# Performance work log

Measured on AMD Instinct MI355X. Metric: run time of the kernel, lower is better.

The kernel has to match this reference:

```python
import jax, jax.numpy as jnp
import numpy as np
from jax import lax

# ---- constants matching init kwargs / proposal_creator(mode='testing') ----
RATIOS = (0.5, 1.0, 2.0)
SCALES = (8.0, 16.0, 32.0)
BASE = 16.0          # generate_anchor_base base_size
STRIDE = 16          # feat_stride
NMS_THRESH = 0.7
N_PRE = 3000         # n_test_pre_nms
N_POST = 300         # n_test_post_nms
MIN_SIZE = 16.0      # min_size * scale (scale=1)


def _anchor_base():
    # (9, 4) xyxy anchors centered at (BASE/2, BASE/2); ratios outer, scales inner
    r = np.array(RATIOS, np.float32)
    s = np.array(SCALES, np.float32)
    hs = (BASE * s[None, :] * np.sqrt(r)[:, None]).reshape(-1)
    ws = (BASE * s[None, :] * np.sqrt(1.0 / r)[:, None]).reshape(-1)
    cx = cy = BASE / 2.0
    return np.stack([cx - ws / 2, cy - hs / 2, cx + ws / 2, cy + hs / 2], 1).astype(np.float32)


def _all_anchors(h, w):
    # _enumerate_shifted_anchor: shift grid flattened y-outer/x-inner to match
    # permute(0,2,3,1).view(n,-1,4) layout of the conv outputs.
    base = jnp.asarray(_anchor_base())                     # (9,4)
    sx = jnp.arange(w, dtype=jnp.float32) * STRIDE
    sy = jnp.arange(h, dtype=jnp.float32) * STRIDE
    SX, SY = jnp.meshgrid(sx, sy)                          # (h,w)
    shifts = jnp.stack([SX, SY, SX, SY], -1).reshape(-1, 4)  # (h*w,4)
    return (shifts[:, None, :] + base[None, :, :]).reshape(-1, 4)  # (h*w*9,4)


def _proposals(loc, score, anchor, img_h, img_w):
    # loc: (K,4) deltas, score: (K,) fg prob, anchor: (K,4) xyxy
    aw = anchor[:, 2] - anchor[:, 0]
    ah = anchor[:, 3] - anchor[:, 1]
    acx = anchor[:, 0] + 0.5 * aw
    acy = anchor[:, 1] + 0.5 * ah
    cx = loc[:, 0] * aw + acx
    cy = loc[:, 1] * ah + acy
    bw = aw * jnp.exp(loc[:, 2])
    bh = ah * jnp.exp(loc[:, 3])
    x1 = jnp.clip(cx - 0.5 * bw, 0.0, img_w)
    y1 = jnp.clip(cy - 0.5 * bh, 0.0, img_h)
    x2 = jnp.clip(cx + 0.5 * bw, 0.0, img_w)
    y2 = jnp.clip(cy + 0.5 * bh, 0.0, img_h)
    boxes = jnp.stack([x1, y1, x2, y2], 1)
    valid = ((x2 - x1) >= MIN_SIZE) & ((y2 - y1) >= MIN_SIZE)
    # min-size filter -> sink invalid boxes with -inf score, then top-k pre-NMS
    masked = jnp.where(valid, score, -jnp.inf)
    _, idx = lax.top_k(masked, N_PRE)
    b = boxes[idx]                                         # (N_PRE,4), score-sorted desc
    v = valid[idx]
    # pairwise IoU (torchvision convention: no +1)
    area = (b[:, 2] - b[:, 0]) * (b[:, 3] - b[:, 1])
    ix1 = jnp.maximum(b[:, None, 0], b[None, :, 0])
    iy1 = jnp.maximum(b[:, None, 1], b[None, :, 1])
    ix2 = jnp.minimum(b[:, None, 2], b[None, :, 2])
    iy2 = jnp.minimum(b[:, None, 3], b[None, :, 3])
    inter = jnp.clip(ix2 - ix1, 0.0) * jnp.clip(iy2 - iy1, 0.0)
    union = area[:, None] + area[None, :] - inter
    iou = jnp.where(union > 0.0, inter / union, 0.0)
    sup = iou > NMS_THRESH                                 # (N_PRE,N_PRE) bool
    # greedy sequential NMS over score order
    ar = jnp.arange(N_PRE)
    def body(keep, i):
        keep = keep & ~(keep[i] & sup[i] & (ar > i))
        return keep, None
    keep, _ = lax.scan(body, v, ar)
    # first N_POST kept boxes (score order); pad by cycling kept boxes
    order = jnp.argsort(jnp.where(keep, ar, N_PRE))        # kept indices first, sorted
    nk = jnp.maximum(keep.sum(), 1)
    pos = jnp.arange(N_POST)
    sel = order[jnp.where(pos < nk, pos, pos % nk)]
    return b[sel]                                          # (N_POST,4)


def setup_inputs() -> dict:
    key = jax.random.key(0)
    ks = jax.random.split(key, 4)
    n, c, h, w = 4, 512, 38, 38
    return {
        "x": jax.random.normal(ks[0], (n, c, h, w), jnp.float32),
        "conv1_w": jax.random.normal(ks[1], (512, 512, 3, 3), jnp.float32) * 0.01,
        "conv1_b": jnp.zeros((512,), jnp.float32),
        "score_w": jax.random.normal(ks[2], (18, 512), jnp.float32) * 0.01,
        "score_b": jnp.zeros((18,), jnp.float32),
        "loc_w": jax.random.normal(ks[3], (36, 512), jnp.float32) * 0.01,
        "loc_b": jnp.zeros((36,), jnp.float32),
        "img_h": 608,
        "img_w": 608,
    }


def reference(x, conv1_w, conv1_b, score_w, score_b, loc_w, loc_b, img_h, img_w):
    n, _, h, w = x.shape
    feat = jax.nn.relu(
        lax.conv_general_dilated(x, conv1_w, (1, 1), "SAME",
                                 dimension_numbers=("NCHW", "OIHW", "NCHW"))
        + conv1_b[None, :, None, None])
    locs = jnp.einsum("nchw,oc->nohw", feat, loc_w) + loc_b[None, :, None, None]
    scores = jnp.einsum("nchw,oc->nohw", feat, score_w) + score_b[None, :, None, None]
    rpn_locs = locs.transpose(0, 2, 3, 1).reshape(n, -1, 4)      # (n, h*w*9, 4)
    rpn_scores = scores.transpose(0, 2, 3, 1).reshape(n, -1, 2)  # (n, h*w*9, 2)
    fg = jax.nn.softmax(rpn_scores, axis=-1)[..., 1]             # (n, h*w*9)
    anchor = _all_anchors(h, w)
    ih = jnp.float32(img_h)
    iw = jnp.float32(img_w)
    rois = jax.vmap(lambda l, s: _proposals(l, s, anchor, ih, iw))(rpn_locs, fg)
    rois_indices = jnp.broadcast_to(
        jnp.arange(n, dtype=x.dtype)[:, None], (n, N_POST))
    return rpn_locs, rpn_scores, rois.reshape(-1, 4), rois_indices, anchor[None]
```

## Files before the change

kernel.cpp:

```cpp
#include <hip/hip_runtime.h>
#include <cstdint>
#include <cstddef>

#define HW    1444
#define NA    12996
#define NPRE  3000
#define NW    47
#define NPOST 300

#define OFF_LOCS   0
#define OFF_SCORES 207936
#define OFF_ROIS   311904
#define OFF_IDX    316704
#define OFF_ANCH   317904

#define INVALID_KEY 0xFFF0000000000000ULL

typedef float f32x2 __attribute__((ext_vector_type(2)));
typedef float f32x4 __attribute__((ext_vector_type(4)));

__device__ inline double as_dim(int raw) {
  if (raw > 0 && raw < 1000000) return (double)raw;
  return (double)__int_as_float(raw);
}

__global__ __launch_bounds__(256) void wt_k(const float* __restrict__ lw,
                                            const float* __restrict__ sw,
                                            float* __restrict__ Wt) {
  int t = blockIdx.x * 256 + threadIdx.x;
  if (t >= 64 * 512) return;
  int o = t & 63, c = t >> 6;
  float v = 0.f;
  if (o < 36)      v = lw[o * 512 + c];
  else if (o < 54) v = sw[(o - 36) * 512 + c];
  Wt[t] = v;
}

__global__ __launch_bounds__(256) void conv_k(const float* __restrict__ X,
                                              const float* __restrict__ W,
                                              const float* __restrict__ B,
                                              float* __restrict__ F) {
  __shared__ float Xs[1008];
  __shared__ float Wsf[2304];
  const int tid  = threadIdx.x;
  const int lane = tid & 63;
  const int wv   = tid >> 6;
  const int seg  = wv * 10;
  const int y  = blockIdx.x;
  const int o0 = blockIdx.y * 64;
  const int n  = blockIdx.z;
  const float* xn = X + ((size_t)n * 512) * HW;

  int xsrcA[2]; bool xvalA[2]; bool xactA1;
  {
    int e = tid;
    int cl = e / 120, rem = e - cl * 120, row = rem / 40, colA = rem - row * 40;
    int m = colA - 1, iy = y - 1 + row;
    xvalA[0] = (m >= 0 && m < 38 && iy >= 0 && iy < 38);
    xsrcA[0] = xvalA[0] ? (cl * HW + iy * 38 + m) : 0;
  }
  {
    int e = tid + 256; xactA1 = (e < 480);
    int cl = e / 120, rem = e - cl * 120, row = rem / 40, colA = rem - row * 40;
    int m = colA - 1, iy = y - 1 + row;
    xvalA[1] = xactA1 && (m >= 0 && m < 38 && iy >= 0 && iy < 38);
    xsrcA[1] = xvalA[1] ? (cl * HW + iy * 38 + m) : 0;
  }
  int xsrcB[3]; bool xvalB[3]; bool xactB2;
#pragma unroll
  for (int u = 0; u < 3; ++u) {
    int e = tid + u * 256;
    bool act = (e < 528);
    int cl = e / 132, rem = e - cl * 132, row = rem / 44, colB = rem - row * 44;
    int m = colB - 3, iy = y - 1 + row;
    xvalB[u] = act && (m >= 0 && m < 38 && iy >= 0 && iy < 38);
    xsrcB[u] = xvalB[u] ? (cl * HW + iy * 38 + m) : 0;
    if (u == 2) xactB2 = act;
  }
  int wsrc[9];
#pragma unroll
  for (int u = 0; u < 9; ++u) {
    int e = tid + u * 256;
    int ol = e / 36, t36 = e - ol * 36;
    wsrc[u] = (o0 + ol) * 4608 + t36;
  }

  float xrA[2], xrB[3], wr_[9];
#pragma unroll
  for (int u = 0; u < 2; ++u) xrA[u] = xvalA[u] ? xn[xsrcA[u]] : 0.f;
#pragma unroll
  for (int u = 0; u < 3; ++u) xrB[u] = xvalB[u] ? xn[xsrcB[u]] : 0.f;
#pragma unroll
  for (int u = 0; u < 9; ++u) wr_[u] = W[wsrc[u]];

  double acc[10];
#pragma unroll
  for (int p = 0; p < 10; ++p) acc[p] = 0.;
  f32x2 pA[5], pB[5];
  float pc0 = 0.f;

  const int  xb0   = (wv & 1) ? (480 + seg + 2) : seg;
  const int  cstep = (wv & 1) ? 132 : 120;
  const int  kstep = (wv & 1) ? 44 : 40;

#define WQ_ELEM(t) ((t & 3) == 0 ? wq[(t) >> 2].x : (t & 3) == 1 ? wq[(t) >> 2].y : \
                    (t & 3) == 2 ? wq[(t) >> 2].z : wq[(t) >> 2].w)

  for (int cc = 0; cc < 128; ++cc) {
    __syncthreads();
    Xs[tid] = xrA[0];
    if (xactA1) Xs[tid + 256] = xrA[1];
    Xs[480 + tid] = xrB[0];
    Xs[480 + tid + 256] = xrB[1];
    if (xactB2) Xs[480 + tid + 512] = xrB[2];
#pragma unroll
    for (int u = 0; u < 9; ++u) Wsf[tid + u * 256] = wr_[u];
    __syncthreads();
    if (cc < 127) {
      const int cb = (cc + 1) * 4;
#pragma unroll
      for (int u = 0; u < 2; ++u) xrA[u] = xvalA[u] ? xn[cb * HW + xsrcA[u]] : 0.f;
#pragma unroll
      for (int u = 0; u < 3; ++u) xrB[u] = xvalB[u] ? xn[cb * HW + xsrcB[u]] : 0.f;
#pragma unroll
      for (int u = 0; u < 9; ++u) wr_[u] = W[wsrc[u] + (cc + 1) * 36];
    }
    f32x4 wq[9];
    {
      const f32x4* wrow = (const f32x4*)&Wsf[lane * 36];
#pragma unroll
      for (int q = 0; q < 9; ++q) wq[q] = wrow[q];
    }
    if ((cc & 1) == 0) {
#pragma unroll
      for (int a = 0; a < 5; ++a) { pA[a] = (f32x2)(0.f); pB[a] = (f32x2)(0.f); }
      pc0 = 0.f;
    }
#pragma unroll
    for (int cl = 0; cl < 4; ++cl) {
      f32x2 wp[9];
#pragma unroll
      for (int k = 0; k < 9; ++k) {
        float wv0 = WQ_ELEM(cl * 9 + k);
        wp[k][0] = wv0; wp[k][1] = wv0;
      }
#pragma unroll
      for (int ky = 0; ky < 3; ++ky) {
        const float* xrow = &Xs[xb0 + cl * cstep + ky * kstep];
        f32x4 q0 = *(const f32x4*)(xrow);
        f32x4 q1 = *(const f32x4*)(xrow + 4);
        f32x4 q2 = *(const f32x4*)(xrow + 8);
        f32x2 xp[6];
        xp[0] = __builtin_shufflevector(q0, q0, 0, 1);
        xp[1] = __builtin_shufflevector(q0, q0, 2, 3);
        xp[2] = __builtin_shufflevector(q1, q1, 0, 1);
        xp[3] = __builtin_shufflevector(q1, q1, 2, 3);
        xp[4] = __builtin_shufflevector(q2, q2, 0, 1);
        xp[5] = __builtin_shufflevector(q2, q2, 2, 3);
#pragma unroll
        for (int a = 0; a < 5; ++a)
          asm("v_pk_fma_f32 %0, %1, %2, %0"
              : "+v"(pA[a]) : "v"(xp[a]), "v"(wp[ky * 3 + 0]));
        pc0 = fmaf(wp[ky * 3 + 1][0], xp[0][1], pc0);
#pragma unroll
        for (int a = 0; a < 5; ++a)
          asm("v_pk_fma_f32 %0, %1, %2, %0"
              : "+v"(pB[a]) : "v"(xp[a + 1]), "v"(wp[ky * 3 + 1]));
#pragma unroll
        for (int a = 0; a < 5; ++a)
          asm("v_pk_fma_f32 %0, %1, %2, %0"
              : "+v"(pA[a]) : "v"(xp[a + 1]), "v"(wp[ky * 3 + 2]));
      }
    }
    if (cc & 1) {
      acc[0] += (double)(pA[0][0] + pc0);
#pragma unroll
      for (int p = 1; p < 10; ++p) {
        float sa = pA[p >> 1][p & 1];
        float sb = (p & 1) ? pB[(p - 1) >> 1][0] : pB[(p - 2) >> 1][1];
        acc[p] += (double)(sa + sb);
      }
    }
  }
  double bb = (double)B[o0 + lane];
  float* fp = F + ((size_t)(n * 512 + o0 + lane)) * HW + y * 38;
#pragma unroll
  for (int p = 0; p < 10; ++p) {
    int col = seg + p;
    if (col < 38) fp[col] = (float)fmax(acc[p] + bb, 0.0);
  }
}

__global__ __launch_bounds__(256) void heads_k(const float* __restrict__ F,
                                               const float* __restrict__ Wt,
                                               const float* __restrict__ lb,
                                               const float* __restrict__ sb,
                                               float* __restrict__ out,
                                               double* __restrict__ fg) {
  __shared__ float sf[512 * 4];
  __shared__ double ssc[4][18];
  int n = blockIdx.y;
  int p0 = blockIdx.x * 4;
  int tid = threadIdx.x;
  const float* fn = F + ((size_t)n * 512) * HW;
  for (int e = tid; e < 2048; e += 256) {
    int c = e >> 2, pl = e & 3;
    sf[e] = fn[c * HW + p0 + pl];
  }
  __syncthreads();
  int pl = tid & 3, o = tid >> 2;
  double acc = 0.;
  if (o < 54) {
    for (int c = 0; c < 512; ++c)
      acc = fma((double)Wt[(c << 6) | o], (double)sf[(c << 2) | pl], acc);
  }
  int p = p0 + pl;
  if (o < 36) {
    acc += (double)lb[o];
    out[OFF_LOCS + ((size_t)n * NA + (size_t)p * 9 + (o >> 2)) * 4 + (o & 3)] = (float)acc;
  } else if (o < 54) {
    int oo = o - 36;
    acc += (double)sb[oo];
    out[OFF_SCORES + ((size_t)n * NA + (size_t)p * 9 + (oo >> 1)) * 2 + (oo & 1)] = (float)acc;
    ssc[pl][oo] = acc;
  }
  __syncthreads();
  if (tid < 36) {
    int pl2 = tid / 9, a = tid - pl2 * 9;
    double s0 = ssc[pl2][a * 2], s1 = ssc[pl2][a * 2 + 1];
    double mx = fmax(s0, s1);
    double e0 = exp(s0 - mx), e1 = exp(s1 - mx);
    fg[(size_t)n * NA + (size_t)(p0 + pl2) * 9 + a] = e1 / (e0 + e1);
  }
}

__global__ __launch_bounds__(256) void decode_k(const float* __restrict__ out_c,
                                                float* __restrict__ out,
                                                const double* __restrict__ fg,
                                                const int* __restrict__ ihp,
                                                const int* __restrict__ iwp,
                                                double* __restrict__ boxes,
                                                unsigned long long* __restrict__ keys) {
  int t = blockIdx.x * 256 + threadIdx.x;
  int n = t >> 14, i = t & 16383;
  if (i >= NA) { keys[t] = ~0ULL; return; }
  int p = i / 9, a = i - p * 9;
  int ri = a / 3, si = a - ri * 3;
  double sr  = (ri == 0) ? 0.7071067811865476 : (ri == 1 ? 1.0 : 1.4142135623730951);
  double sri = (ri == 0) ? 1.4142135623730951 : (ri == 1 ? 1.0 : 0.7071067811865476);
  double hs = (double)(128 << si) * sr;
  double wd = (double)(128 << si) * sri;
  int py = p / 38, px = p - py * 38;
  float sx = (float)(px * 16), sy = (float)(py * 16);
  float fx1 = (float)(8.0 - 0.5 * wd), fy1 = (float)(8.0 - 0.5 * hs);
  float fx2 = (float)(8.0 + 0.5 * wd), fy2 = (float)(8.0 + 0.5 * hs);
  float ax1f = sx + fx1, ay1f = sy + fy1, ax2f = sx + fx2, ay2f = sy + fy2;
  if (n == 0) {
    float* ap = out + OFF_ANCH + (size_t)i * 4;
    ap[0] = ax1f; ap[1] = ay1f; ap[2] = ax2f; ap[3] = ay2f;
  }
  double ax1 = ax1f, ay1 = ay1f, ax2 = ax2f, ay2 = ay2f;
  double aw = ax2 - ax1, ah = ay2 - ay1;
  double acx = ax1 + 0.5 * aw, acy = ay1 + 0.5 * ah;
  const float* lp = out_c + OFF_LOCS + ((size_t)n * NA + i) * 4;
  double cx = (double)lp[0] * aw + acx, cy = (double)lp[1] * ah + acy;
  double bw = aw * exp((double)lp[2]), bh = ah * exp((double)lp[3]);
  double iwf = as_dim(iwp[0]), ihf = as_dim(ihp[0]);
  double x1 = fmin(fmax(cx - 0.5 * bw, 0.0), iwf);
  double y1 = fmin(fmax(cy - 0.5 * bh, 0.0), ihf);
  double x2 = fmin(fmax(cx + 0.5 * bw, 0.0), iwf);
  double y2 = fmin(fmax(cy + 0.5 * bh, 0.0), ihf);
  bool valid = ((x2 - x1) >= 16.0) && ((y2 - y1) >= 16.0);
  double* bp = boxes + ((size_t)n * NA + i) * 4;
  bp[0] = x1; bp[1] = y1; bp[2] = x2; bp[3] = y2;
  double sc = fg[(size_t)n * NA + i];
  unsigned long long u = (unsigned long long)__double_as_longlong(sc);
  u = (u >> 63) ? ~u : (u | 0x8000000000000000ULL);
  unsigned long long inv = ~u;
  if (!valid) inv = INVALID_KEY;
  keys[t] = (inv & ~0x3FFFULL) | (unsigned long long)i;
}

__global__ __launch_bounds__(1024) void sortA_k(unsigned long long* __restrict__ keys) {
  __shared__ unsigned long long s[8192];
  const int half = blockIdx.x & 1;
  unsigned long long* g = keys + (((size_t)(blockIdx.x >> 1)) << 14) + ((size_t)half << 13);
  const int tid = threadIdx.x;
  for (int i = tid; i < 8192; i += 1024) s[i] = g[i];
  for (int size = 2; size <= 8192; size <<= 1) {
    for (int stride = size >> 1; stride > 0; stride >>= 1) {
      __syncthreads();
      for (int u = tid; u < 4096; u += 1024) {
        int lo = u & (stride - 1);
        int i1 = ((u - lo) << 1) | lo;
        int i2 = i1 + stride;
        bool up = (i1 & size) == 0;
        if (half) up = !up;
        unsigned long long a = s[i1], b = s[i2];
        if ((a > b) == up) { s[i1] = b; s[i2] = a; }
      }
    }
  }
  __syncthreads();
  for (int i = tid; i < 8192; i += 1024) g[i] = s[i];
}

__global__ __launch_bounds__(256) void sortB_k(unsigned long long* __restrict__ keys) {
  int t = blockIdx.x * 256 + threadIdx.x;
  int n = t >> 13, i = t & 8191;
  unsigned long long* g = keys + ((size_t)n << 14);
  unsigned long long a = g[i], b = g[i + 8192];
  if (a > b) { g[i] = b; g[i + 8192] = a; }
}

__global__ __launch_bounds__(1024) void sortC_k(unsigned long long* __restrict__ keys) {
  __shared__ unsigned long long s[8192];
  unsigned long long* g = keys + (((size_t)(blockIdx.x >> 1)) << 14) + ((size_t)(blockIdx.x & 1) << 13);
  const int tid = threadIdx.x;
  for (int i = tid; i < 8192; i += 1024) s[i] = g[i];
  for (int stride = 4096; stride > 0; stride >>= 1) {
    __syncthreads();
    for (int u = tid; u < 4096; u += 1024) {
      int lo = u & (stride - 1);
      int i1 = ((u - lo) << 1) | lo;
      int i2 = i1 + stride;
      unsigned long long a = s[i1], b = s[i2];
      if (a > b) { s[i1] = b; s[i2] = a; }
    }
  }
  __syncthreads();
  for (int i = tid; i < 8192; i += 1024) g[i] = s[i];
}

__global__ void gather_k(const unsigned long long* __restrict__ keys,
                         const double* __restrict__ boxes,
                         double* __restrict__ bsort,
                         unsigned long long* __restrict__ vw) {
  int n = blockIdx.y, w = blockIdx.x, l = threadIdx.x;
  int r = w * 64 + l;
  bool valid = false;
  if (r < NPRE) {
    unsigned long long kk = keys[((size_t)n << 14) + r];
    valid = kk < INVALID_KEY;
    unsigned idx = (unsigned)(kk & 0x3FFFULL);
    const double* bp = boxes + ((size_t)n * NA + idx) * 4;
    double* dp = bsort + ((size_t)n * NPRE + r) * 4;
    dp[0] = bp[0]; dp[1] = bp[1]; dp[2] = bp[2]; dp[3] = bp[3];
  }
  unsigned long long mask = __ballot(valid);
  if (l == 0) vw[n * NW + w] = mask;
}

__global__ __launch_bounds__(256) void iou_k(const double* __restrict__ bsort,
                                             unsigned long long* __restrict__ sup) {
  int t = blockIdx.x * 256 + threadIdx.x;
  if (t >= 4 * NPRE * NW) return;
  int w = t % NW; int rest = t / NW; int i = rest % NPRE; int n = rest / NPRE;
  const double* bb = bsort + (size_t)n * NPRE * 4;
  double bix1 = bb[(size_t)i*4], biy1 = bb[(size_t)i*4+1];
  double bix2 = bb[(size_t)i*4+2], biy2 = bb[(size_t)i*4+3];
  double ai = (bix2 - bix1) * (biy2 - biy1);
  unsigned long long word = 0ULL;
  int j0 = w << 6;
  if (j0 + 63 > i) {
    int lmax = NPRE - j0; if (lmax > 64) lmax = 64;
    for (int l = 0; l < lmax; ++l) {
      int j = j0 + l;
      if (j <= i) continue;
      const double* bj = bb + (size_t)j * 4;
      double aj = (bj[2] - bj[0]) * (bj[3] - bj[1]);
      double xx1 = fmax(bix1, bj[0]), yy1 = fmax(biy1, bj[1]);
      double xx2 = fmin(bix2, bj[2]), yy2 = fmin(biy2, bj[3]);
      double inter = fmax(xx2 - xx1, 0.0) * fmax(yy2 - yy1, 0.0);
      double uni = ai + aj - inter;
      double iou = (uni > 0.0) ? inter / uni : 0.0;
      word |= (unsigned long long)(iou > 0.7) << l;
    }
  }
  sup[((size_t)n * NPRE + i) * NW + w] = word;
}

__global__ void nms_k(const unsigned long long* __restrict__ sup,
                      const unsigned long long* __restrict__ vwp,
                      const double* __restrict__ bsort,
                      float* __restrict__ out) {
  int n = blockIdx.x; int l = threadIdx.x;
  unsigned long long vw = (l < NW) ? vwp[n * NW + l] : 0ULL;
  unsigned long long remv = 0ULL, keepw = 0ULL;
  const unsigned long long* sbase = sup + (size_t)n * NPRE * NW;
  unsigned long long r = (l < NPRE) ? sbase[(size_t)l * NW] : 0ULL;
  for (int b = 0; b < NW; ++b) {
    unsigned long long rn = 0ULL;
    if (b + 1 < NW) {
      int gi = (b + 1) * 64 + l;
      if (gi < NPRE) rn = sbase[(size_t)gi * NW + (b + 1)];
    }
    unsigned long long kept = __shfl(vw & ~remv, b);
    unsigned long long todo = kept;
    while (todo) {
      int i = __builtin_ctzll(todo);
      unsigned long long ri = __shfl(r, i);
      kept &= ~ri;
      todo &= todo - 1;
      todo &= ~ri;
    }
    if (l == b) keepw = kept;
    unsigned long long m = kept;
    while (m) {
      int i0 = __builtin_ctzll(m); m &= m - 1;
      int i1 = -1, i2 = -1, i3 = -1, i4 = -1, i5 = -1, i6 = -1, i7 = -1;
      if (m) { i1 = __builtin_ctzll(m); m &= m - 1; }
      if (m) { i2 = __builtin_ctzll(m); m &= m - 1; }
      if (m) { i3 = __builtin_ctzll(m); m &= m - 1; }
      if (m) { i4 = __builtin_ctzll(m); m &= m - 1; }
      if (m) { i5 = __builtin_ctzll(m); m &= m - 1; }
      if (m) { i6 = __builtin_ctzll(m); m &= m - 1; }
      if (m) { i7 = __builtin_ctzll(m); m &= m - 1; }
      if (l < NW) {
        const unsigned long long* rb = sbase + (size_t)(b << 6) * NW + l;
        unsigned long long a0 = rb[(size_t)i0 * NW];
        unsigned long long a1 = (i1 >= 0) ? rb[(size_t)i1 * NW] : 0ULL;
        unsigned long long a2 = (i2 >= 0) ? rb[(size_t)i2 * NW] : 0ULL;
        unsigned long long a3 = (i3 >= 0) ? rb[(size_t)i3 * NW] : 0ULL;
        unsigned long long a4 = (i4 >= 0) ? rb[(size_t)i4 * NW] : 0ULL;
        unsigned long long a5 = (i5 >= 0) ? rb[(size_t)i5 * NW] : 0ULL;
        unsigned long long a6 = (i6 >= 0) ? rb[(size_t)i6 * NW] : 0ULL;
        unsigned long long a7 = (i7 >= 0) ? rb[(size_t)i7 * NW] : 0ULL;
        remv |= (((a0 | a1) | (a2 | a3)) | ((a4 | a5) | (a6 | a7)));
      }
    }
    r = rn;
  }
  unsigned long long keep = keepw;
  int cnt = __popcll(keep);
  int pre = cnt;
#pragma unroll
  for (int d = 1; d < 64; d <<= 1) {
    int tt = __shfl_up(pre, d);
    if (l >= d) pre += tt;
  }
  int nk = __shfl(pre, 63);
  int excl = pre - cnt;
  __shared__ float sbox[NPOST * 4];
  unsigned long long m2 = keep; int rank = excl;
  while (m2) {
    int b = __builtin_ctzll(m2);
    m2 &= m2 - 1;
    if (rank < NPOST) {
      int j = (l << 6) + b;
      const double* bj = bsort + ((size_t)n * NPRE + j) * 4;
      sbox[rank*4]   = (float)bj[0]; sbox[rank*4+1] = (float)bj[1];
      sbox[rank*4+2] = (float)bj[2]; sbox[rank*4+3] = (float)bj[3];
    }
    ++rank;
  }
  __syncthreads();
  if (nk == 0 && l == 0) {
    const double* b0 = bsort + (size_t)n * NPRE * 4;
    sbox[0] = (float)b0[0]; sbox[1] = (float)b0[1];
    sbox[2] = (float)b0[2]; sbox[3] = (float)b0[3];
  }
  __syncthreads();
  int nke = nk > 0 ? nk : 1;
  for (int r2 = l; r2 < NPOST; r2 += 64) {
    int src = r2 < nke ? r2 : r2 % nke;
    float4 b4 = *(float4*)(sbox + src * 4);
    *(float4*)(out + OFF_ROIS + ((size_t)n * NPOST + r2) * 4) = b4;
    out[OFF_IDX + n * NPOST + r2] = (float)n;
  }
}

extern "C" void kernel_launch(void* const* d_in, const int* in_sizes, int n_in,
                              void* d_out, int out_size, void* d_ws, size_t ws_size,
                              hipStream_t stream) {
  const float* X  = (const float*)d_in[0];
  const float* CW = (const float*)d_in[1];
  const float* CB = (const float*)d_in[2];
  const float* SW = (const float*)d_in[3];
  const float* SB = (const float*)d_in[4];
  const float* LW = (const float*)d_in[5];
  const float* LB = (const float*)d_in[6];
  const int*   IH = (const int*)d_in[7];
  const int*   IW = (const int*)d_in[8];
  float* out = (float*)d_out;
  char* ws = (char*)d_ws;

  float* feat = (float*)(ws + 0);
  unsigned long long* sup  = (unsigned long long*)(ws + 0);
  float* Wt    = (float*)(ws + 11829248);
  double* fg   = (double*)(ws + 11960320);
  double* boxes= (double*)(ws + 12376192);
  unsigned long long* keys = (unsigned long long*)(ws + 14039680);
  double* bsort= (double*)(ws + 14563968);
  unsigned long long* vw   = (unsigned long long*)(ws + 14947968);

  hipLaunchKernelGGL(wt_k,     dim3(128),        dim3(256),  0, stream, LW, SW, Wt);
  hipLaunchKernelGGL(conv_k,   dim3(38, 8, 4),   dim3(256),  0, stream, X, CW, CB, feat);
  hipLaunchKernelGGL(heads_k,  dim3(361, 4),     dim3(256),  0, stream, feat, Wt, LB, SB, out, fg);
  hipLaunchKernelGGL(decode_k, dim3(256),        dim3(256),  0, stream, out, out, fg, IH, IW, boxes, keys);
  hipLaunchKernelGGL(sortA_k,  dim3(8),          dim3(1024), 0, stream, keys);
  hipLaunchKernelGGL(sortB_k,  dim3(128),        dim3(256),  0, stream, keys);
  hipLaunchKernelGGL(sortC_k,  dim3(8),          dim3(1024), 0, stream, keys);
  hipLaunchKernelGGL(gather_k, dim3(47, 4),      dim3(64),   0, stream, keys, boxes, bsort, vw);
  hipLaunchKernelGGL(iou_k,    dim3((4*NPRE*NW + 255) / 256), dim3(256), 0, stream, bsort, sup);
  hipLaunchKernelGGL(nms_k,    dim3(4),          dim3(64),   0, stream, sup, vw, bsort, out);
}
```

Baseline: 980.2 us.

## Fuse decode into heads, merge sort stages with gather, drop IoU division

The box decode and key generation now run in the heads kernel's epilogue, reading locs from shared memory instead of launching a separate decode kernel. Key padding moves into the weight-transpose kernel. The bitonic merge step, final half-sort and gather are combined into one kernel: it keeps only the smaller half of each merged pair, sorts it, and gathers the top boxes from shared memory. The IoU test compares inter against 0.7*union instead of dividing, which removes launches and global round trips but can flip results in rare rounding edge cases. The fused sort runs only 4 blocks, which may limit parallelism.

Result: no change. 968.6 us (-1.2%).

```diff
diff --git a/kernel.cpp b/kernel.cpp
--- a/kernel.cpp
+++ b/kernel.cpp
@@ -26,8 +26,13 @@
 
 __global__ __launch_bounds__(256) void wt_k(const float* __restrict__ lw,
                                             const float* __restrict__ sw,
-                                            float* __restrict__ Wt) {
+                                            float* __restrict__ Wt,
+                                            unsigned long long* __restrict__ keys) {
   int t = blockIdx.x * 256 + threadIdx.x;
+  if (t < 4 * (16384 - NA)) {
+    int n2 = t / (16384 - NA), r = t - n2 * (16384 - NA);
+    keys[((size_t)n2 << 14) + NA + r] = ~0ULL;
+  }
   if (t >= 64 * 512) return;
   int o = t & 63, c = t >> 6;
   float v = 0.f;
@@ -195,10 +200,14 @@
                                                const float* __restrict__ Wt,
                                                const float* __restrict__ lb,
                                                const float* __restrict__ sb,
+                                               const int* __restrict__ ihp,
+                                               const int* __restrict__ iwp,
                                                float* __restrict__ out,
-                                               double* __restrict__ fg) {
+                                               double* __restrict__ boxes,
+                                               unsigned long long* __restrict__ keys) {
   __shared__ float sf[512 * 4];
   __shared__ double ssc[4][18];
+  __shared__ float sloc[4][36];
   int n = blockIdx.y;
   int p0 = blockIdx.x * 4;
   int tid = threadIdx.x;
@@ -217,7 +226,9 @@
   int p = p0 + pl;
   if (o < 36) {
     acc += (double)lb[o];
-    out[OFF_LOCS + ((size_t)n * NA + (size_t)p * 9 + (o >> 2)) * 4 + (o & 3)] = (float)acc;
+    float v = (float)acc;
+    out[OFF_LOCS + ((size_t)n * NA + (size_t)p * 9 + (o >> 2)) * 4 + (o & 3)] = v;
+    sloc[pl][o] = v;
   } else if (o < 54) {
     int oo = o - 36;
     acc += (double)sb[oo];
@@ -230,55 +241,44 @@
     double s0 = ssc[pl2][a * 2], s1 = ssc[pl2][a * 2 + 1];
     double mx = fmax(s0, s1);
     double e0 = exp(s0 - mx), e1 = exp(s1 - mx);
-    fg[(size_t)n * NA + (size_t)(p0 + pl2) * 9 + a] = e1 / (e0 + e1);
-  }
-}
-
-__global__ __launch_bounds__(256) void decode_k(const float* __restrict__ out_c,
-                                                float* __restrict__ out,
-                                                const double* __restrict__ fg,
-                                                const int* __restrict__ ihp,
-                                                const int* __restrict__ iwp,
-                                                double* __restrict__ boxes,
-                                                unsigned long long* __restrict__ keys) {
-  int t = blockIdx.x * 256 + threadIdx.x;
-  int n = t >> 14, i = t & 16383;
-  if (i >= NA) { keys[t] = ~0ULL; return; }
-  int p = i / 9, a = i - p * 9;
-  int ri = a / 3, si = a - ri * 3;
-  double sr  = (ri == 0) ? 0.7071067811865476 : (ri == 1 ? 1.0 : 1.4142135623730951);
-  double sri = (ri == 0) ? 1.4142135623730951 : (ri == 1 ? 1.0 : 0.7071067811865476);
-  double hs = (double)(128 << si) * sr;
-  double wd = (double)(128 << si) * sri;
-  int py = p / 38, px = p - py * 38;
-  float sx = (float)(px * 16), sy = (float)(py * 16);
-  float fx1 = (float)(8.0 - 0.5 * wd), fy1 = (float)(8.0 - 0.5 * hs);
-  float fx2 = (float)(8.0 + 0.5 * wd), fy2 = (float)(8.0 + 0.5 * hs);
-  float ax1f = sx + fx1, ay1f = sy + fy1, ax2f = sx + fx2, ay2f = sy + fy2;
-  if (n == 0) {
-    float* ap = out + OFF_ANCH + (size_t)i * 4;
-    ap[0] = ax1f; ap[1] = ay1f; ap[2] = ax2f; ap[3] = ay2f;
-  }
-  double ax1 = ax1f, ay1 = ay1f, ax2 = ax2f, ay2 = ay2f;
-  double aw = ax2 - ax1, ah = ay2 - ay1;
-  double acx = ax1 + 0.5 * aw, acy = ay1 + 0.5 * ah;
-  const float* lp = out_c + OFF_LOCS + ((size_t)n * NA + i) * 4;
-  double cx = (double)lp[0] * aw + acx, cy = (double)lp[1] * ah + acy;
-  double bw = aw * exp((double)lp[2]), bh = ah * exp((double)lp[3]);
-  double iwf = as_dim(iwp[0]), ihf = as_dim(ihp[0]);
-  double x1 = fmin(fmax(cx - 0.5 * bw, 0.0), iwf);
-  double y1 = fmin(fmax(cy - 0.5 * bh, 0.0), ihf);
-  double x2 = fmin(fmax(cx + 0.5 * bw, 0.0), iwf);
-  double y2 = fmin(fmax(cy + 0.5 * bh, 0.0), ihf);
-  bool valid = ((x2 - x1) >= 16.0) && ((y2 - y1) >= 16.0);
-  double* bp = boxes + ((size_t)n * NA + i) * 4;
-  bp[0] = x1; bp[1] = y1; bp[2] = x2; bp[3] = y2;
-  double sc = fg[(size_t)n * NA + i];
-  unsigned long long u = (unsigned long long)__double_as_longlong(sc);
-  u = (u >> 63) ? ~u : (u | 0x8000000000000000ULL);
-  unsigned long long inv = ~u;
-  if (!valid) inv = INVALID_KEY;
-  keys[t] = (inv & ~0x3FFFULL) | (unsigned long long)i;
+    double sc = e1 / (e0 + e1);
+    int pp = p0 + pl2;
+    int i = pp * 9 + a;
+    int ri = a / 3, si = a - ri * 3;
+    double sr  = (ri == 0) ? 0.7071067811865476 : (ri == 1 ? 1.0 : 1.4142135623730951);
+    double sri = (ri == 0) ? 1.4142135623730951 : (ri == 1 ? 1.0 : 0.7071067811865476);
+    double hs = (double)(128 << si) * sr;
+    double wd = (double)(128 << si) * sri;
+    int py = pp / 38, px = pp - py * 38;
+    float sx = (float)(px * 16), sy = (float)(py * 16);
+    float fx1 = (float)(8.0 - 0.5 * wd), fy1 = (float)(8.0 - 0.5 * hs);
+    float fx2 = (float)(8.0 + 0.5 * wd), fy2 = (float)(8.0 + 0.5 * hs);
+    float ax1f = sx + fx1, ay1f = sy + fy1, ax2f = sx + fx2, ay2f = sy + fy2;
+    if (n == 0) {
+      float* ap = out + OFF_ANCH + (size_t)i * 4;
+      ap[0] = ax1f; ap[1] = ay1f; ap[2] = ax2f; ap[3] = ay2f;
+    }
+    double ax1 = ax1f, ay1 = ay1f, ax2 = ax2f, ay2 = ay2f;
+    double aw = ax2 - ax1, ah = ay2 - ay1;
+    double acx = ax1 + 0.5 * aw, acy = ay1 + 0.5 * ah;
+    double l0 = (double)sloc[pl2][a * 4 + 0], l1 = (double)sloc[pl2][a * 4 + 1];
+    double l2 = (double)sloc[pl2][a * 4 + 2], l3 = (double)sloc[pl2][a * 4 + 3];
+    double cx = l0 * aw + acx, cy = l1 * ah + acy;
+    double bw = aw * exp(l2), bh = ah * exp(l3);
+    double iwf = as_dim(iwp[0]), ihf = as_dim(ihp[0]);
+    double x1 = fmin(fmax(cx - 0.5 * bw, 0.0), iwf);
+    double y1 = fmin(fmax(cy - 0.5 * bh, 0.0), ihf);
+    double x2 = fmin(fmax(cx + 0.5 * bw, 0.0), iwf);
+    double y2 = fmin(fmax(cy + 0.5 * bh, 0.0), ihf);
+    bool valid = ((x2 - x1) >= 16.0) && ((y2 - y1) >= 16.0);
+    double* bp = boxes + ((size_t)n * NA + i) * 4;
+    bp[0] = x1; bp[1] = y1; bp[2] = x2; bp[3] = y2;
+    unsigned long long u = (unsigned long long)__double_as_longlong(sc);
+    u = (u >> 63) ? ~u : (u | 0x8000000000000000ULL);
+    unsigned long long inv = ~u;
+    if (!valid) inv = INVALID_KEY;
+    keys[((size_t)n << 14) + i] = (inv & ~0x3FFFULL) | (unsigned long long)i;
+  }
 }
 
 __global__ __launch_bounds__(1024) void sortA_k(unsigned long long* __restrict__ keys) {
@@ -305,19 +305,18 @@
   for (int i = tid; i < 8192; i += 1024) g[i] = s[i];
 }
 
-__global__ __launch_bounds__(256) void sortB_k(unsigned long long* __restrict__ keys) {
-  int t = blockIdx.x * 256 + threadIdx.x;
-  int n = t >> 13, i = t & 8191;
-  unsigned long long* g = keys + ((size_t)n << 14);
-  unsigned long long a = g[i], b = g[i + 8192];
-  if (a > b) { g[i] = b; g[i + 8192] = a; }
-}
-
-__global__ __launch_bounds__(1024) void sortC_k(unsigned long long* __restrict__ keys) {
+__global__ __launch_bounds__(1024) void sortCG_k(const unsigned long long* __restrict__ keys,
+                                                 const double* __restrict__ boxes,
+                                                 double* __restrict__ bsort,
+                                                 unsigned long long* __restrict__ vw) {
   __shared__ unsigned long long s[8192];
-  unsigned long long* g = keys + (((size_t)(blockIdx.x >> 1)) << 14) + ((size_t)(blockIdx.x & 1) << 13);
+  const int n = blockIdx.x;
+  const unsigned long long* g = keys + ((size_t)n << 14);
   const int tid = threadIdx.x;
-  for (int i = tid; i < 8192; i += 1024) s[i] = g[i];
+  for (int i = tid; i < 8192; i += 1024) {
+    unsigned long long a = g[i], b = g[i + 8192];
+    s[i] = a < b ? a : b;
+  }
   for (int stride = 4096; stride > 0; stride >>= 1) {
     __syncthreads();
     for (int u = tid; u < 4096; u += 1024) {
@@ -329,26 +328,23 @@
     }
   }
   __syncthreads();
-  for (int i = tid; i < 8192; i += 1024) g[i] = s[i];
-}
-
-__global__ void gather_k(const unsigned long long* __restrict__ keys,
-                         const double* __restrict__ boxes,
-                         double* __restrict__ bsort,
-                         unsigned long long* __restrict__ vw) {
-  int n = blockIdx.y, w = blockIdx.x, l = threadIdx.x;
-  int r = w * 64 + l;
-  bool valid = false;
-  if (r < NPRE) {
-    unsigned long long kk = keys[((size_t)n << 14) + r];
-    valid = kk < INVALID_KEY;
-    unsigned idx = (unsigned)(kk & 0x3FFFULL);
-    const double* bp = boxes + ((size_t)n * NA + idx) * 4;
-    double* dp = bsort + ((size_t)n * NPRE + r) * 4;
-    dp[0] = bp[0]; dp[1] = bp[1]; dp[2] = bp[2]; dp[3] = bp[3];
-  }
-  unsigned long long mask = __ballot(valid);
-  if (l == 0) vw[n * NW + w] = mask;
+  const int lane = tid & 63;
+#pragma unroll
+  for (int r3 = 0; r3 < 3; ++r3) {
+    int r = r3 * 1024 + tid;
+    bool valid = false;
+    if (r < NPRE) {
+      unsigned long long kk = s[r];
+      valid = kk < INVALID_KEY;
+      unsigned idx = (unsigned)(kk & 0x3FFFULL);
+      const double* bp = boxes + ((size_t)n * NA + idx) * 4;
+      double* dp = bsort + ((size_t)n * NPRE + r) * 4;
+      dp[0] = bp[0]; dp[1] = bp[1]; dp[2] = bp[2]; dp[3] = bp[3];
+    }
+    unsigned long long mask = __ballot(valid);
+    int w = r >> 6;
+    if (lane == 0 && w < NW) vw[n * NW + w] = mask;
+  }
 }
 
 __global__ __launch_bounds__(256) void iou_k(const double* __restrict__ bsort,
@@ -373,8 +369,8 @@
       double xx2 = fmin(bix2, bj[2]), yy2 = fmin(biy2, bj[3]);
       double inter = fmax(xx2 - xx1, 0.0) * fmax(yy2 - yy1, 0.0);
       double uni = ai + aj - inter;
-      double iou = (uni > 0.0) ? inter / uni : 0.0;
-      word |= (unsigned long long)(iou > 0.7) << l;
+      bool supb = (uni > 0.0) && (inter > 0.7 * uni);
+      word |= (unsigned long long)supb << l;
     }
   }
   sup[((size_t)n * NPRE + i) * NW + w] = word;
@@ -488,20 +484,17 @@
   float* feat = (float*)(ws + 0);
   unsigned long long* sup  = (unsigned long long*)(ws + 0);
   float* Wt    = (float*)(ws + 11829248);
-  double* fg   = (double*)(ws + 11960320);
   double* boxes= (double*)(ws + 12376192);
   unsigned long long* keys = (unsigned long long*)(ws + 14039680);
   double* bsort= (double*)(ws + 14563968);
   unsigned long long* vw   = (unsigned long long*)(ws + 14947968);
 
-  hipLaunchKernelGGL(wt_k,     dim3(128),        dim3(256),  0, stream, LW, SW, Wt);
-  hipLaunchKernelGGL(conv_k,   dim3(38, 8, 4),   dim3(256),  0, stream, X, CW, CB, feat);
-  hipLaunchKernelGGL(heads_k,  dim3(361, 4),     dim3(256),  0, stream, feat, Wt, LB, SB, out, fg);
-  hipLaunchKernelGGL(decode_k, dim3(256),        dim3(256),  0, stream, out, out, fg, IH, IW, boxes, keys);
-  hipLaunchKernelGGL(sortA_k,  dim3(8),          dim3(1024), 0, stream, keys);
-  hipLaunchKernelGGL(sortB_k,  dim3(128),        dim3(256),  0, stream, keys);
-  hipLaunchKernelGGL(sortC_k,  dim3(8),          dim3(1024), 0, stream, keys);
-  hipLaunchKernelGGL(gather_k, dim3(47, 4),      dim3(64),   0, stream, keys, boxes, bsort, vw);
-  hipLaunchKernelGGL(iou_k,    dim3((4*NPRE*NW + 255) / 256), dim3(256), 0, stream, bsort, sup);
-  hipLaunchKernelGGL(nms_k,    dim3(4),          dim3(64),   0, stream, sup, vw, bsort, out);
-}
+  hipLaunchKernelGGL(wt_k,    dim3(128),      dim3(256),  0, stream, LW, SW, Wt, keys);
+  hipLaunchKernelGGL(conv_k,  dim3(38, 8, 4), dim3(256),  0, stream, X, CW, CB, feat);
+  hipLaunchKernelGGL(heads_k, dim3(361, 4),   dim3(256),  0, stream,
+                     feat, Wt, LB, SB, IH, IW, out, boxes, keys);
+  hipLaunchKernelGGL(sortA_k, dim3(8),        dim3(1024), 0, stream, keys);
+  hipLaunchKernelGGL(sortCG_k,dim3(4),        dim3(1024), 0, stream, keys, boxes, bsort, vw);
+  hipLaunchKernelGGL(iou_k,   dim3((4*NPRE*NW + 255) / 256), dim3(256), 0, stream, bsort, sup);
+  hipLaunchKernelGGL(nms_k,   dim3(4),        dim3(64),   0, stream, sup, vw, bsort, out);
+}
```
